# Kernel optimization log

Measured on AMD Instinct MI355X. Metric: run time of the kernel, lower is better.

The kernel has to match this reference:

```python
import jax, jax.numpy as jnp
import numpy as np

B, T, I, H = 256, 1024, 128, 256


def setup_inputs() -> dict:
    key = jax.random.key(0)
    ks = jax.random.split(key, 10)
    p = lambda k, shape: jax.random.normal(k, shape, dtype=jnp.float32) * 0.1
    return {
        "x": jax.random.normal(ks[0], (B, T, I), dtype=jnp.float32),
        # forget gate
        "f_wh": p(ks[1], (H, H)), "f_wx": p(ks[2], (I, H)), "f_b": p(ks[3], (H,)),
        # input (create) gate: potential (tanh) and percent (sigmoid) branches
        "i_wh_pot": p(ks[4], (H, H)), "i_wx_pot": p(ks[5], (I, H)), "i_b_pot": p(ks[6], (H,)),
        "i_wh_perc": p(ks[7], (H, H)), "i_wx_perc": p(ks[8], (I, H)), "i_b_perc": p(ks[9], (H,)),
        # output gate
        "o_wh": p(jax.random.fold_in(key, 10), (H, H)),
        "o_wx": p(jax.random.fold_in(key, 11), (I, H)),
        "o_b": p(jax.random.fold_in(key, 12), (H,)),
    }


def reference(x, f_wh, f_wx, f_b, i_wh_pot, i_wx_pot, i_b_pot,
              i_wh_perc, i_wx_perc, i_b_perc, o_wh, o_wx, o_b):
    # x: [B, T, I]
    sigmoid, tanh = jax.nn.sigmoid, jnp.tanh

    def step(carry, xt):  # xt: [B, I]
        s, l = carry  # short_term [B,H], long_term [B,H]
        forget = sigmoid(s @ f_wh + xt @ f_wx + f_b)
        create = sigmoid(s @ i_wh_perc + xt @ i_wx_perc + i_b_perc) * \
                 tanh(s @ i_wh_pot + xt @ i_wx_pot + i_b_pot)
        l_new = forget * l + create
        s_new = tanh(l_new) * sigmoid(s @ o_wh + xt @ o_wx + o_b)
        return (s_new, l_new), None

    init = (jnp.zeros((x.shape[0], f_b.shape[0]), x.dtype),
            jnp.zeros((x.shape[0], f_b.shape[0]), x.dtype))
    (short_term, long_term), _ = jax.lax.scan(step, init, jnp.swapaxes(x, 0, 1))
    return short_term, long_term
```

## Files before the change

### kernel.cpp

```cpp
#include <hip/hip_runtime.h>
#include <cstdint>

#define T_STEPS 1024
#define I_DIM 128
#define H_DIM 256

typedef __attribute__((ext_vector_type(8))) short bf16x8;
typedef __attribute__((ext_vector_type(4))) float f32x4;
typedef __attribute__((ext_vector_type(2))) unsigned int u32x2;

__device__ __forceinline__ uint32_t f2bf(float f) {
    uint32_t u = __builtin_bit_cast(uint32_t, f);
    return (u + 0x7FFFu + ((u >> 16) & 1u)) >> 16;
}
__device__ __forceinline__ uint32_t pk2bf(float lo, float hi) {
    return (f2bf(lo) & 0xFFFFu) | (f2bf(hi) << 16);
}
__device__ __forceinline__ float sigmoid_(float v) { return 1.f / (1.f + __expf(-v)); }
__device__ __forceinline__ float tanh_(float v) { float e = __expf(2.f * v); return 1.f - 2.f / (e + 1.f); }

__device__ __forceinline__ void barrier_lgkm() {
    asm volatile("s_waitcnt lgkmcnt(0)\n\ts_barrier" ::: "memory");
}

__global__ void __launch_bounds__(256, 1)
lstm_kernel(const float* __restrict__ x,
            const float* __restrict__ f_wh, const float* __restrict__ f_wx, const float* __restrict__ f_b,
            const float* __restrict__ p_wh, const float* __restrict__ p_wx, const float* __restrict__ p_b,
            const float* __restrict__ c_wh, const float* __restrict__ c_wx, const float* __restrict__ c_b,
            const float* __restrict__ o_wh, const float* __restrict__ o_wx, const float* __restrict__ o_b,
            float* __restrict__ out, uint8_t* __restrict__ ws)
{
    __shared__ __align__(16) uint8_t lds[65792];
    uint8_t* WH = lds;
    uint8_t* WX = lds + 32768;
    uint8_t* SL = lds + 49152;
    uint8_t* XT = lds + 57344;
    float*   GB = (float*)(lds + 61440);

    const int tid  = (int)threadIdx.x;
    const int lane = tid & 63;
    const int wv   = tid >> 6;
    const int blk  = (int)blockIdx.x;
    const int grp  = blk & 15;
    const int cwg  = blk >> 4;
    const int grow0 = grp << 4;
    const int hc0   = cwg << 4;

    uint8_t* sbase = ws + 4096;

    const float* wh = (wv == 0) ? f_wh : (wv == 1) ? p_wh : (wv == 2) ? c_wh : o_wh;
    const float* wx = (wv == 0) ? f_wx : (wv == 1) ? p_wx : (wv == 2) ? c_wx : o_wx;
    const float* bp = (wv == 0) ? f_b  : (wv == 1) ? p_b  : (wv == 2) ? c_b  : o_b;

    {
        const int col = lane & 15, kc = lane >> 4;
        const uint32_t csw = (uint32_t)((col & 7) << 4);
        uint8_t* whb = WH + (size_t)(wv * 16 + col) * 512;
        #pragma unroll
        for (int it = 0; it < 8; ++it) {
            const int k0 = it * 32 + kc * 8;
            float v0 = wh[(size_t)(k0 + 0) * H_DIM + hc0 + col];
            float v1 = wh[(size_t)(k0 + 1) * H_DIM + hc0 + col];
            float v2 = wh[(size_t)(k0 + 2) * H_DIM + hc0 + col];
            float v3 = wh[(size_t)(k0 + 3) * H_DIM + hc0 + col];
            float v4 = wh[(size_t)(k0 + 4) * H_DIM + hc0 + col];
            float v5 = wh[(size_t)(k0 + 5) * H_DIM + hc0 + col];
            float v6 = wh[(size_t)(k0 + 6) * H_DIM + hc0 + col];
            float v7 = wh[(size_t)(k0 + 7) * H_DIM + hc0 + col];
            uint4 pk;
            pk.x = pk2bf(v0, v1); pk.y = pk2bf(v2, v3);
            pk.z = pk2bf(v4, v5); pk.w = pk2bf(v6, v7);
            *(uint4*)(whb + (((uint32_t)(it * 64 + kc * 16)) ^ csw)) = pk;
        }
        uint8_t* wxb = WX + (size_t)(wv * 16 + col) * 256;
        #pragma unroll
        for (int it = 0; it < 4; ++it) {
            const int k0 = it * 32 + kc * 8;
            float v0 = wx[(size_t)(k0 + 0) * H_DIM + hc0 + col];
            float v1 = wx[(size_t)(k0 + 1) * H_DIM + hc0 + col];
            float v2 = wx[(size_t)(k0 + 2) * H_DIM + hc0 + col];
            float v3 = wx[(size_t)(k0 + 3) * H_DIM + hc0 + col];
            float v4 = wx[(size_t)(k0 + 4) * H_DIM + hc0 + col];
            float v5 = wx[(size_t)(k0 + 5) * H_DIM + hc0 + col];
            float v6 = wx[(size_t)(k0 + 6) * H_DIM + hc0 + col];
            float v7 = wx[(size_t)(k0 + 7) * H_DIM + hc0 + col];
            uint4 pk;
            pk.x = pk2bf(v0, v1); pk.y = pk2bf(v2, v3);
            pk.z = pk2bf(v4, v5); pk.w = pk2bf(v6, v7);
            *(uint4*)(wxb + (((uint32_t)(it * 64 + kc * 16)) ^ csw)) = pk;
        }
    }
    const float bias = bp[hc0 + (lane & 15)];
    __syncthreads();

    const int fr = lane & 15, fkc = lane >> 4;
    const uint32_t fsw = (uint32_t)((fr & 7) << 4);
    uint8_t* slA = SL + (size_t)fr * 512;
    uint8_t* xtA = XT + (size_t)fr * 256;
    const uint8_t* whB = WH + (size_t)(wv * 16 + fr) * 512;
    const uint8_t* wxB = WX + (size_t)(wv * 16 + fr) * 256;

    uint4 bwh[8], bwx[4];
    #pragma unroll
    for (int q = 0; q < 8; ++q)
        bwh[q] = *(const uint4*)(whB + (((uint32_t)(q * 64 + fkc * 16)) ^ fsw));
    #pragma unroll
    for (int q = 0; q < 4; ++q)
        bwx[q] = *(const uint4*)(wxB + (((uint32_t)(q * 64 + fkc * 16)) ^ fsw));

    const int crow = tid >> 4, ccol = tid & 15;
    const size_t pub_off = (size_t)(grow0 + crow) * 1024 + (size_t)(cwg * 8 + (ccol >> 1)) * 8;

    if ((tid & 1) == 0) {
        u32x2 pd; pd.x = 0u; pd.y = 1u;
        asm volatile("global_store_dwordx2 %0, %1, off sc0 sc1" :: "v"(sbase + pub_off), "v"(pd) : "memory");
    }
    asm volatile("s_barrier" ::: "memory");
    if (tid == 0) {
        const uint32_t h = 1u;
        asm volatile("global_store_dword %0, %1, off sc0 sc1"
                     :: "v"(ws + (size_t)grp * 64 + (size_t)cwg * 4), "v"(h) : "memory");
    }

    const int xrow = tid >> 4, xseg = tid & 15;
    const uint32_t xsw = (uint32_t)((xrow & 7) << 4);
    const float* xptr = x + (size_t)(grow0 + xrow) * (T_STEPS * I_DIM) + xseg * 8;
    float4 xr0 = *(const float4*)(xptr);
    float4 xr1 = *(const float4*)(xptr + 4);

    const size_t poll_off = (size_t)(grow0 + xrow) * 1024 + (size_t)xseg * 64;
    const uint8_t* hintp = ws + (size_t)grp * 64 + (size_t)xseg * 4;

    float l_reg = 0.f, s_fin = 0.f, l_fin = 0.f;

    for (int t = 0; t < T_STEPS; ++t) {
        {
            uint4 pk;
            pk.x = pk2bf(xr0.x, xr0.y); pk.y = pk2bf(xr0.z, xr0.w);
            pk.z = pk2bf(xr1.x, xr1.y); pk.w = pk2bf(xr1.z, xr1.w);
            *(uint4*)(XT + (size_t)xrow * 256 + (((uint32_t)(xseg * 16)) ^ xsw)) = pk;
        }
        {
            const int tn = (t + 1 < T_STEPS) ? (t + 1) : (T_STEPS - 1);
            const float* p = xptr + (size_t)tn * I_DIM;
            xr0 = *(const float4*)(p);
            xr1 = *(const float4*)(p + 4);
        }
        barrier_lgkm();

        const uint32_t e = (uint32_t)t + 1u;
        {
            uint32_t h;
            for (;;) {
                asm volatile("global_load_dword %0, %1, off sc0 sc1"
                             : "=v"(h) : "v"(hintp) : "memory");
                asm volatile("s_waitcnt vmcnt(0)" ::: "memory");
                __builtin_amdgcn_sched_barrier(0);
                if (__all(h >= e)) break;
            }
        }

        uint4 g0, g1, g2, g3;
        const size_t par = (size_t)((t & 1) ? 262144 : 0);
        const uint8_t* src = sbase + par + poll_off;
        asm volatile("global_load_dwordx4 %0, %1, off sc0 sc1" : "=v"(g0) : "v"(src) : "memory");
        asm volatile("global_load_dwordx4 %0, %1, off offset:16 sc0 sc1" : "=v"(g1) : "v"(src) : "memory");
        asm volatile("global_load_dwordx4 %0, %1, off offset:32 sc0 sc1" : "=v"(g2) : "v"(src) : "memory");
        asm volatile("global_load_dwordx4 %0, %1, off offset:48 sc0 sc1" : "=v"(g3) : "v"(src) : "memory");

        f32x4 accA = {0.f, 0.f, 0.f, 0.f};
        #pragma unroll
        for (int q = 0; q < 4; ++q) {
            uint4 av = *(const uint4*)(xtA + (((uint32_t)(q * 64 + fkc * 16)) ^ fsw));
            accA = __builtin_amdgcn_mfma_f32_16x16x32_bf16(
                __builtin_bit_cast(bf16x8, av), __builtin_bit_cast(bf16x8, bwx[q]), accA, 0, 0, 0);
        }

        asm volatile("s_waitcnt vmcnt(0)" ::: "memory");
        __builtin_amdgcn_sched_barrier(0);
        {
            uint32_t m = (g0.y ^ e) | (g0.w ^ e) | (g1.y ^ e) | (g1.w ^ e)
                       | (g2.y ^ e) | (g2.w ^ e) | (g3.y ^ e) | (g3.w ^ e);
            while (m != 0) {
                asm volatile("global_load_dwordx4 %0, %1, off sc0 sc1" : "=v"(g0) : "v"(src) : "memory");
                asm volatile("global_load_dwordx4 %0, %1, off offset:16 sc0 sc1" : "=v"(g1) : "v"(src) : "memory");
                asm volatile("global_load_dwordx4 %0, %1, off offset:32 sc0 sc1" : "=v"(g2) : "v"(src) : "memory");
                asm volatile("global_load_dwordx4 %0, %1, off offset:48 sc0 sc1" : "=v"(g3) : "v"(src) : "memory");
                asm volatile("s_waitcnt vmcnt(0)" ::: "memory");
                __builtin_amdgcn_sched_barrier(0);
                m = (g0.y ^ e) | (g0.w ^ e) | (g1.y ^ e) | (g1.w ^ e)
                  | (g2.y ^ e) | (g2.w ^ e) | (g3.y ^ e) | (g3.w ^ e);
            }
        }

        {
            uint4 d0; d0.x = g0.x; d0.y = g0.z; d0.z = g1.x; d0.w = g1.z;
            uint4 d1; d1.x = g2.x; d1.y = g2.z; d1.z = g3.x; d1.w = g3.z;
            uint8_t* dst = SL + (size_t)xrow * 512;
            const uint32_t o = (uint32_t)(xseg * 32);
            *(uint4*)(dst + (o ^ xsw)) = d0;
            *(uint4*)(dst + ((o + 16) ^ xsw)) = d1;
        }
        barrier_lgkm();

        f32x4 accB = {0.f, 0.f, 0.f, 0.f};
        #pragma unroll
        for (int q = 0; q < 4; ++q) {
            uint4 a0 = *(const uint4*)(slA + (((uint32_t)(q * 64 + fkc * 16)) ^ fsw));
            uint4 a1 = *(const uint4*)(slA + (((uint32_t)((q + 4) * 64 + fkc * 16)) ^ fsw));
            accA = __builtin_amdgcn_mfma_f32_16x16x32_bf16(
                __builtin_bit_cast(bf16x8, a0), __builtin_bit_cast(bf16x8, bwh[q]), accA, 0, 0, 0);
            accB = __builtin_amdgcn_mfma_f32_16x16x32_bf16(
                __builtin_bit_cast(bf16x8, a1), __builtin_bit_cast(bf16x8, bwh[q + 4]), accB, 0, 0, 0);
        }

        #pragma unroll
        for (int j = 0; j < 4; ++j) {
            const float pre = accA[j] + accB[j] + bias;
            const float a = (wv == 1) ? tanh_(pre) : sigmoid_(pre);
            GB[wv * 272 + (fkc * 4 + j) * 17 + fr] = a;
        }
        barrier_lgkm();

        {
            const float fg  = GB[0 * 272 + crow * 17 + ccol];
            const float pot = GB[1 * 272 + crow * 17 + ccol];
            const float prc = GB[2 * 272 + crow * 17 + ccol];
            const float og  = GB[3 * 272 + crow * 17 + ccol];
            const float lnew = fg * l_reg + prc * pot;
            const float snew = tanh_(lnew) * og;
            l_reg = lnew;
            if (t == T_STEPS - 1) { s_fin = snew; l_fin = lnew; }
            const uint32_t sb = f2bf(snew);
            const uint32_t ob = (uint32_t)__shfl_xor((int)sb, 1, 64);
            if (((tid & 1) == 0) && (t != T_STEPS - 1)) {
                const size_t po = (size_t)(((t + 1) & 1) ? 262144 : 0) + pub_off;
                u32x2 pd; pd.x = (sb & 0xFFFFu) | (ob << 16); pd.y = (uint32_t)t + 2u;
                asm volatile("global_store_dwordx2 %0, %1, off sc0 sc1" :: "v"(sbase + po), "v"(pd) : "memory");
            }
        }
        if (t != T_STEPS - 1) {
            asm volatile("s_barrier" ::: "memory");
            if (tid == 0) {
                const uint32_t h = (uint32_t)t + 2u;
                asm volatile("global_store_dword %0, %1, off sc0 sc1"
                             :: "v"(ws + (size_t)grp * 64 + (size_t)cwg * 4), "v"(h) : "memory");
            }
        }
    }

    out[(size_t)(grow0 + crow) * H_DIM + hc0 + ccol] = s_fin;
    out[(size_t)H_DIM * H_DIM + (size_t)(grow0 + crow) * H_DIM + hc0 + ccol] = l_fin;
}

extern "C" void kernel_launch(void* const* d_in, const int* in_sizes, int n_in,
                              void* d_out, int out_size, void* d_ws, size_t ws_size,
                              hipStream_t stream) {
    const float* x    = (const float*)d_in[0];
    const float* f_wh = (const float*)d_in[1];
    const float* f_wx = (const float*)d_in[2];
    const float* f_b  = (const float*)d_in[3];
    const float* p_wh = (const float*)d_in[4];
    const float* p_wx = (const float*)d_in[5];
    const float* p_b  = (const float*)d_in[6];
    const float* c_wh = (const float*)d_in[7];
    const float* c_wx = (const float*)d_in[8];
    const float* c_b  = (const float*)d_in[9];
    const float* o_wh = (const float*)d_in[10];
    const float* o_wx = (const float*)d_in[11];
    const float* o_b  = (const float*)d_in[12];
    float* outp = (float*)d_out;
    uint8_t* wsp = (uint8_t*)d_ws;

    hipMemsetAsync(d_ws, 0, 4096 + 2 * 262144, stream);

    void* args[] = { (void*)&x,
                     (void*)&f_wh, (void*)&f_wx, (void*)&f_b,
                     (void*)&p_wh, (void*)&p_wx, (void*)&p_b,
                     (void*)&c_wh, (void*)&c_wx, (void*)&c_b,
                     (void*)&o_wh, (void*)&o_wx, (void*)&o_b,
                     (void*)&outp, (void*)&wsp };
    hipLaunchCooperativeKernel((const void*)lstm_kernel, dim3(256), dim3(256), args, 0, stream);
}
```

Measured before the change: 2.410 ms.

## Process two 16-row batch groups per block, halving grid and dropping hint flag polling

Each block now handles 32 batch rows as two interleaved 16-row sub-groups (A and B), with the grid halved to 128 blocks and block-to-group mapping changed. The per-group hint flag store/poll is removed; consumers spin directly on the epoch tags embedded in the published state. LDS is reused by overlaying state/x buffers onto the weight staging area after weights are loaded into registers. This lets sub-group B's exchange latency overlap sub-group A's compute, at the cost of serializing two sub-steps per timestep within each block.

After: 3.965 ms. 64.5% more time.

```diff
diff --git a/kernel.cpp b/kernel.cpp
--- a/kernel.cpp
+++ b/kernel.cpp
@@ -31,20 +31,22 @@
             const float* __restrict__ o_wh, const float* __restrict__ o_wx, const float* __restrict__ o_b,
             float* __restrict__ out, uint8_t* __restrict__ ws)
 {
-    __shared__ __align__(16) uint8_t lds[65792];
-    uint8_t* WH = lds;
-    uint8_t* WX = lds + 32768;
-    uint8_t* SL = lds + 49152;
-    uint8_t* XT = lds + 57344;
-    float*   GB = (float*)(lds + 61440);
+    __shared__ __align__(16) uint8_t lds[49152];
+    uint8_t* WH  = lds;
+    uint8_t* WX  = lds + 32768;
+    uint8_t* SLa = lds;
+    uint8_t* SLb = lds + 8192;
+    uint8_t* XTa = lds + 16384;
+    uint8_t* XTb = lds + 20480;
+    float*   GB  = (float*)(lds + 24576);
 
     const int tid  = (int)threadIdx.x;
     const int lane = tid & 63;
     const int wv   = tid >> 6;
     const int blk  = (int)blockIdx.x;
-    const int grp  = blk & 15;
-    const int cwg  = blk >> 4;
-    const int grow0 = grp << 4;
+    const int grp  = blk >> 4;
+    const int cwg  = blk & 15;
+    const int grow0 = grp << 5;
     const int hc0   = cwg << 4;
 
     uint8_t* sbase = ws + 4096;
@@ -96,8 +98,10 @@
 
     const int fr = lane & 15, fkc = lane >> 4;
     const uint32_t fsw = (uint32_t)((fr & 7) << 4);
-    uint8_t* slA = SL + (size_t)fr * 512;
-    uint8_t* xtA = XT + (size_t)fr * 256;
+    uint8_t* slAa = SLa + (size_t)fr * 512;
+    uint8_t* slAb = SLb + (size_t)fr * 512;
+    uint8_t* xtAa = XTa + (size_t)fr * 256;
+    uint8_t* xtAb = XTb + (size_t)fr * 256;
     const uint8_t* whB = WH + (size_t)(wv * 16 + fr) * 512;
     const uint8_t* wxB = WX + (size_t)(wv * 16 + fr) * 256;
 
@@ -108,78 +112,75 @@
     #pragma unroll
     for (int q = 0; q < 4; ++q)
         bwx[q] = *(const uint4*)(wxB + (((uint32_t)(q * 64 + fkc * 16)) ^ fsw));
+    __syncthreads();
 
     const int crow = tid >> 4, ccol = tid & 15;
-    const size_t pub_off = (size_t)(grow0 + crow) * 1024 + (size_t)(cwg * 8 + (ccol >> 1)) * 8;
+    const size_t pub_offA = (size_t)(grow0 + crow) * 1024 + (size_t)(cwg * 8 + (ccol >> 1)) * 8;
+    const size_t pub_offB = pub_offA + 16384;
 
     if ((tid & 1) == 0) {
         u32x2 pd; pd.x = 0u; pd.y = 1u;
-        asm volatile("global_store_dwordx2 %0, %1, off sc0 sc1" :: "v"(sbase + pub_off), "v"(pd) : "memory");
-    }
-    asm volatile("s_barrier" ::: "memory");
-    if (tid == 0) {
-        const uint32_t h = 1u;
-        asm volatile("global_store_dword %0, %1, off sc0 sc1"
-                     :: "v"(ws + (size_t)grp * 64 + (size_t)cwg * 4), "v"(h) : "memory");
+        asm volatile("global_store_dwordx2 %0, %1, off sc0 sc1" :: "v"(sbase + pub_offA), "v"(pd) : "memory");
+        asm volatile("global_store_dwordx2 %0, %1, off sc0 sc1" :: "v"(sbase + pub_offB), "v"(pd) : "memory");
     }
 
     const int xrow = tid >> 4, xseg = tid & 15;
     const uint32_t xsw = (uint32_t)((xrow & 7) << 4);
-    const float* xptr = x + (size_t)(grow0 + xrow) * (T_STEPS * I_DIM) + xseg * 8;
-    float4 xr0 = *(const float4*)(xptr);
-    float4 xr1 = *(const float4*)(xptr + 4);
-
-    const size_t poll_off = (size_t)(grow0 + xrow) * 1024 + (size_t)xseg * 64;
-    const uint8_t* hintp = ws + (size_t)grp * 64 + (size_t)xseg * 4;
-
-    float l_reg = 0.f, s_fin = 0.f, l_fin = 0.f;
+    const float* xptrA = x + (size_t)(grow0 + xrow) * (T_STEPS * I_DIM) + xseg * 8;
+    const float* xptrB = x + (size_t)(grow0 + 16 + xrow) * (T_STEPS * I_DIM) + xseg * 8;
+    float4 xa0 = *(const float4*)(xptrA);
+    float4 xa1 = *(const float4*)(xptrA + 4);
+    float4 xb0 = *(const float4*)(xptrB);
+    float4 xb1 = *(const float4*)(xptrB + 4);
+
+    const size_t poll_offA = (size_t)(grow0 + xrow) * 1024 + (size_t)xseg * 64;
+    const size_t poll_offB = poll_offA + 16384;
+
+    float l_regA = 0.f, l_regB = 0.f;
+    float s_finA = 0.f, l_finA = 0.f, s_finB = 0.f, l_finB = 0.f;
 
     for (int t = 0; t < T_STEPS; ++t) {
+        const uint32_t e = (uint32_t)t + 1u;
+        const size_t par  = (size_t)((t & 1) ? 262144 : 0);
+        const size_t parn = (size_t)(((t + 1) & 1) ? 262144 : 0);
+
         {
             uint4 pk;
-            pk.x = pk2bf(xr0.x, xr0.y); pk.y = pk2bf(xr0.z, xr0.w);
-            pk.z = pk2bf(xr1.x, xr1.y); pk.w = pk2bf(xr1.z, xr1.w);
-            *(uint4*)(XT + (size_t)xrow * 256 + (((uint32_t)(xseg * 16)) ^ xsw)) = pk;
+            pk.x = pk2bf(xa0.x, xa0.y); pk.y = pk2bf(xa0.z, xa0.w);
+            pk.z = pk2bf(xa1.x, xa1.y); pk.w = pk2bf(xa1.z, xa1.w);
+            *(uint4*)(XTa + (size_t)xrow * 256 + (((uint32_t)(xseg * 16)) ^ xsw)) = pk;
+            pk.x = pk2bf(xb0.x, xb0.y); pk.y = pk2bf(xb0.z, xb0.w);
+            pk.z = pk2bf(xb1.x, xb1.y); pk.w = pk2bf(xb1.z, xb1.w);
+            *(uint4*)(XTb + (size_t)xrow * 256 + (((uint32_t)(xseg * 16)) ^ xsw)) = pk;
         }
         {
             const int tn = (t + 1 < T_STEPS) ? (t + 1) : (T_STEPS - 1);
-            const float* p = xptr + (size_t)tn * I_DIM;
-            xr0 = *(const float4*)(p);
-            xr1 = *(const float4*)(p + 4);
-        }
-        barrier_lgkm();
-
-        const uint32_t e = (uint32_t)t + 1u;
-        {
-            uint32_t h;
-            for (;;) {
-                asm volatile("global_load_dword %0, %1, off sc0 sc1"
-                             : "=v"(h) : "v"(hintp) : "memory");
-                asm volatile("s_waitcnt vmcnt(0)" ::: "memory");
-                __builtin_amdgcn_sched_barrier(0);
-                if (__all(h >= e)) break;
-            }
-        }
+            const float* pA = xptrA + (size_t)tn * I_DIM;
+            const float* pB = xptrB + (size_t)tn * I_DIM;
+            xa0 = *(const float4*)(pA); xa1 = *(const float4*)(pA + 4);
+            xb0 = *(const float4*)(pB); xb1 = *(const float4*)(pB + 4);
+        }
+        barrier_lgkm();
 
         uint4 g0, g1, g2, g3;
-        const size_t par = (size_t)((t & 1) ? 262144 : 0);
-        const uint8_t* src = sbase + par + poll_off;
-        asm volatile("global_load_dwordx4 %0, %1, off sc0 sc1" : "=v"(g0) : "v"(src) : "memory");
-        asm volatile("global_load_dwordx4 %0, %1, off offset:16 sc0 sc1" : "=v"(g1) : "v"(src) : "memory");
-        asm volatile("global_load_dwordx4 %0, %1, off offset:32 sc0 sc1" : "=v"(g2) : "v"(src) : "memory");
-        asm volatile("global_load_dwordx4 %0, %1, off offset:48 sc0 sc1" : "=v"(g3) : "v"(src) : "memory");
-
+        {
+            const uint8_t* src = sbase + par + poll_offA;
+            asm volatile("global_load_dwordx4 %0, %1, off sc0 sc1" : "=v"(g0) : "v"(src) : "memory");
+            asm volatile("global_load_dwordx4 %0, %1, off offset:16 sc0 sc1" : "=v"(g1) : "v"(src) : "memory");
+            asm volatile("global_load_dwordx4 %0, %1, off offset:32 sc0 sc1" : "=v"(g2) : "v"(src) : "memory");
+            asm volatile("global_load_dwordx4 %0, %1, off offset:48 sc0 sc1" : "=v"(g3) : "v"(src) : "memory");
+        }
         f32x4 accA = {0.f, 0.f, 0.f, 0.f};
         #pragma unroll
         for (int q = 0; q < 4; ++q) {
-            uint4 av = *(const uint4*)(xtA + (((uint32_t)(q * 64 + fkc * 16)) ^ fsw));
+            uint4 av = *(const uint4*)(xtAa + (((uint32_t)(q * 64 + fkc * 16)) ^ fsw));
             accA = __builtin_amdgcn_mfma_f32_16x16x32_bf16(
                 __builtin_bit_cast(bf16x8, av), __builtin_bit_cast(bf16x8, bwx[q]), accA, 0, 0, 0);
         }
-
         asm volatile("s_waitcnt vmcnt(0)" ::: "memory");
         __builtin_amdgcn_sched_barrier(0);
         {
+            const uint8_t* src = sbase + par + poll_offA;
             uint32_t m = (g0.y ^ e) | (g0.w ^ e) | (g1.y ^ e) | (g1.w ^ e)
                        | (g2.y ^ e) | (g2.w ^ e) | (g3.y ^ e) | (g3.w ^ e);
             while (m != 0) {
@@ -193,65 +194,134 @@
                   | (g2.y ^ e) | (g2.w ^ e) | (g3.y ^ e) | (g3.w ^ e);
             }
         }
-
         {
             uint4 d0; d0.x = g0.x; d0.y = g0.z; d0.z = g1.x; d0.w = g1.z;
             uint4 d1; d1.x = g2.x; d1.y = g2.z; d1.z = g3.x; d1.w = g3.z;
-            uint8_t* dst = SL + (size_t)xrow * 512;
+            uint8_t* dst = SLa + (size_t)xrow * 512;
             const uint32_t o = (uint32_t)(xseg * 32);
             *(uint4*)(dst + (o ^ xsw)) = d0;
             *(uint4*)(dst + ((o + 16) ^ xsw)) = d1;
         }
         barrier_lgkm();
-
-        f32x4 accB = {0.f, 0.f, 0.f, 0.f};
-        #pragma unroll
-        for (int q = 0; q < 4; ++q) {
-            uint4 a0 = *(const uint4*)(slA + (((uint32_t)(q * 64 + fkc * 16)) ^ fsw));
-            uint4 a1 = *(const uint4*)(slA + (((uint32_t)((q + 4) * 64 + fkc * 16)) ^ fsw));
-            accA = __builtin_amdgcn_mfma_f32_16x16x32_bf16(
-                __builtin_bit_cast(bf16x8, a0), __builtin_bit_cast(bf16x8, bwh[q]), accA, 0, 0, 0);
-            accB = __builtin_amdgcn_mfma_f32_16x16x32_bf16(
-                __builtin_bit_cast(bf16x8, a1), __builtin_bit_cast(bf16x8, bwh[q + 4]), accB, 0, 0, 0);
-        }
-
-        #pragma unroll
-        for (int j = 0; j < 4; ++j) {
-            const float pre = accA[j] + accB[j] + bias;
-            const float a = (wv == 1) ? tanh_(pre) : sigmoid_(pre);
-            GB[wv * 272 + (fkc * 4 + j) * 17 + fr] = a;
-        }
-        barrier_lgkm();
-
+        {
+            f32x4 accB = {0.f, 0.f, 0.f, 0.f};
+            #pragma unroll
+            for (int q = 0; q < 4; ++q) {
+                uint4 a0 = *(const uint4*)(slAa + (((uint32_t)(q * 64 + fkc * 16)) ^ fsw));
+                uint4 a1 = *(const uint4*)(slAa + (((uint32_t)((q + 4) * 64 + fkc * 16)) ^ fsw));
+                accA = __builtin_amdgcn_mfma_f32_16x16x32_bf16(
+                    __builtin_bit_cast(bf16x8, a0), __builtin_bit_cast(bf16x8, bwh[q]), accA, 0, 0, 0);
+                accB = __builtin_amdgcn_mfma_f32_16x16x32_bf16(
+                    __builtin_bit_cast(bf16x8, a1), __builtin_bit_cast(bf16x8, bwh[q + 4]), accB, 0, 0, 0);
+            }
+            #pragma unroll
+            for (int j = 0; j < 4; ++j) {
+                const float pre = accA[j] + accB[j] + bias;
+                const float a = (wv == 1) ? tanh_(pre) : sigmoid_(pre);
+                GB[wv * 272 + (fkc * 4 + j) * 17 + fr] = a;
+            }
+        }
+        barrier_lgkm();
         {
             const float fg  = GB[0 * 272 + crow * 17 + ccol];
             const float pot = GB[1 * 272 + crow * 17 + ccol];
             const float prc = GB[2 * 272 + crow * 17 + ccol];
             const float og  = GB[3 * 272 + crow * 17 + ccol];
-            const float lnew = fg * l_reg + prc * pot;
+            const float lnew = fg * l_regA + prc * pot;
             const float snew = tanh_(lnew) * og;
-            l_reg = lnew;
-            if (t == T_STEPS - 1) { s_fin = snew; l_fin = lnew; }
+            l_regA = lnew;
+            if (t == T_STEPS - 1) { s_finA = snew; l_finA = lnew; }
             const uint32_t sb = f2bf(snew);
             const uint32_t ob = (uint32_t)__shfl_xor((int)sb, 1, 64);
             if (((tid & 1) == 0) && (t != T_STEPS - 1)) {
-                const size_t po = (size_t)(((t + 1) & 1) ? 262144 : 0) + pub_off;
                 u32x2 pd; pd.x = (sb & 0xFFFFu) | (ob << 16); pd.y = (uint32_t)t + 2u;
-                asm volatile("global_store_dwordx2 %0, %1, off sc0 sc1" :: "v"(sbase + po), "v"(pd) : "memory");
-            }
-        }
-        if (t != T_STEPS - 1) {
-            asm volatile("s_barrier" ::: "memory");
-            if (tid == 0) {
-                const uint32_t h = (uint32_t)t + 2u;
-                asm volatile("global_store_dword %0, %1, off sc0 sc1"
-                             :: "v"(ws + (size_t)grp * 64 + (size_t)cwg * 4), "v"(h) : "memory");
+                asm volatile("global_store_dwordx2 %0, %1, off sc0 sc1"
+                             :: "v"(sbase + parn + pub_offA), "v"(pd) : "memory");
+            }
+        }
+
+        {
+            const uint8_t* src = sbase + par + poll_offB;
+            asm volatile("global_load_dwordx4 %0, %1, off sc0 sc1" : "=v"(g0) : "v"(src) : "memory");
+            asm volatile("global_load_dwordx4 %0, %1, off offset:16 sc0 sc1" : "=v"(g1) : "v"(src) : "memory");
+            asm volatile("global_load_dwordx4 %0, %1, off offset:32 sc0 sc1" : "=v"(g2) : "v"(src) : "memory");
+            asm volatile("global_load_dwordx4 %0, %1, off offset:48 sc0 sc1" : "=v"(g3) : "v"(src) : "memory");
+        }
+        f32x4 accC = {0.f, 0.f, 0.f, 0.f};
+        #pragma unroll
+        for (int q = 0; q < 4; ++q) {
+            uint4 av = *(const uint4*)(xtAb + (((uint32_t)(q * 64 + fkc * 16)) ^ fsw));
+            accC = __builtin_amdgcn_mfma_f32_16x16x32_bf16(
+                __builtin_bit_cast(bf16x8, av), __builtin_bit_cast(bf16x8, bwx[q]), accC, 0, 0, 0);
+        }
+        asm volatile("s_waitcnt vmcnt(0)" ::: "memory");
+        __builtin_amdgcn_sched_barrier(0);
+        {
+            const uint8_t* src = sbase + par + poll_offB;
+            uint32_t m = (g0.y ^ e) | (g0.w ^ e) | (g1.y ^ e) | (g1.w ^ e)
+                       | (g2.y ^ e) | (g2.w ^ e) | (g3.y ^ e) | (g3.w ^ e);
+            while (m != 0) {
+                asm volatile("global_load_dwordx4 %0, %1, off sc0 sc1" : "=v"(g0) : "v"(src) : "memory");
+                asm volatile("global_load_dwordx4 %0, %1, off offset:16 sc0 sc1" : "=v"(g1) : "v"(src) : "memory");
+                asm volatile("global_load_dwordx4 %0, %1, off offset:32 sc0 sc1" : "=v"(g2) : "v"(src) : "memory");
+                asm volatile("global_load_dwordx4 %0, %1, off offset:48 sc0 sc1" : "=v"(g3) : "v"(src) : "memory");
+                asm volatile("s_waitcnt vmcnt(0)" ::: "memory");
+                __builtin_amdgcn_sched_barrier(0);
+                m = (g0.y ^ e) | (g0.w ^ e) | (g1.y ^ e) | (g1.w ^ e)
+                  | (g2.y ^ e) | (g2.w ^ e) | (g3.y ^ e) | (g3.w ^ e);
+            }
+        }
+        {
+            uint4 d0; d0.x = g0.x; d0.y = g0.z; d0.z = g1.x; d0.w = g1.z;
+            uint4 d1; d1.x = g2.x; d1.y = g2.z; d1.z = g3.x; d1.w = g3.z;
+            uint8_t* dst = SLb + (size_t)xrow * 512;
+            const uint32_t o = (uint32_t)(xseg * 32);
+            *(uint4*)(dst + (o ^ xsw)) = d0;
+            *(uint4*)(dst + ((o + 16) ^ xsw)) = d1;
+        }
+        barrier_lgkm();
+        {
+            f32x4 accD = {0.f, 0.f, 0.f, 0.f};
+            #pragma unroll
+            for (int q = 0; q < 4; ++q) {
+                uint4 a0 = *(const uint4*)(slAb + (((uint32_t)(q * 64 + fkc * 16)) ^ fsw));
+                uint4 a1 = *(const uint4*)(slAb + (((uint32_t)((q + 4) * 64 + fkc * 16)) ^ fsw));
+                accC = __builtin_amdgcn_mfma_f32_16x16x32_bf16(
+                    __builtin_bit_cast(bf16x8, a0), __builtin_bit_cast(bf16x8, bwh[q]), accC, 0, 0, 0);
+                accD = __builtin_amdgcn_mfma_f32_16x16x32_bf16(
+                    __builtin_bit_cast(bf16x8, a1), __builtin_bit_cast(bf16x8, bwh[q + 4]), accD, 0, 0, 0);
+            }
+            #pragma unroll
+            for (int j = 0; j < 4; ++j) {
+                const float pre = accC[j] + accD[j] + bias;
+                const float a = (wv == 1) ? tanh_(pre) : sigmoid_(pre);
+                GB[wv * 272 + (fkc * 4 + j) * 17 + fr] = a;
+            }
+        }
+        barrier_lgkm();
+        {
+            const float fg  = GB[0 * 272 + crow * 17 + ccol];
+            const float pot = GB[1 * 272 + crow * 17 + ccol];
+            const float prc = GB[2 * 272 + crow * 17 + ccol];
+            const float og  = GB[3 * 272 + crow * 17 + ccol];
+            const float lnew = fg * l_regB + prc * pot;
+            const float snew = tanh_(lnew) * og;
+            l_regB = lnew;
+            if (t == T_STEPS - 1) { s_finB = snew; l_finB = lnew; }
+            const uint32_t sb = f2bf(snew);
+            const uint32_t ob = (uint32_t)__shfl_xor((int)sb, 1, 64);
+            if (((tid & 1) == 0) && (t != T_STEPS - 1)) {
+                u32x2 pd; pd.x = (sb & 0xFFFFu) | (ob << 16); pd.y = (uint32_t)t + 2u;
+                asm volatile("global_store_dwordx2 %0, %1, off sc0 sc1"
+                             :: "v"(sbase + parn + pub_offB), "v"(pd) : "memory");
             }
         }
     }
 
-    out[(size_t)(grow0 + crow) * H_DIM + hc0 + ccol] = s_fin;
-    out[(size_t)H_DIM * H_DIM + (size_t)(grow0 + crow) * H_DIM + hc0 + ccol] = l_fin;
+    out[(size_t)(grow0 + crow) * H_DIM + hc0 + ccol] = s_finA;
+    out[(size_t)H_DIM * H_DIM + (size_t)(grow0 + crow) * H_DIM + hc0 + ccol] = l_finA;
+    out[(size_t)(grow0 + 16 + crow) * H_DIM + hc0 + ccol] = s_finB;
+    out[(size_t)H_DIM * H_DIM + (size_t)(grow0 + 16 + crow) * H_DIM + hc0 + ccol] = l_finB;
 }
 
 extern "C" void kernel_launch(void* const* d_in, const int* in_sizes, int n_in,
@@ -281,5 +351,5 @@
                      (void*)&c_wh, (void*)&c_wx, (void*)&c_b,
                      (void*)&o_wh, (void*)&o_wx, (void*)&o_b,
                      (void*)&outp, (void*)&wsp };
-    hipLaunchCooperativeKernel((const void*)lstm_kernel, dim3(256), dim3(256), args, 0, stream);
-}
+    hipLaunchCooperativeKernel((const void*)lstm_kernel, dim3(128), dim3(256), args, 0, stream);
+}
```
